# Performance work log

Measured on AMD Instinct MI355X. Metric: run time of the kernel, lower is better.

The kernel has to match this reference:

```python
import jax, jax.numpy as jnp
import numpy as np
import itertools

BINS_NUM = 35
BINS_SIZE = 9
ORDERS = (2, 3, 4, 5)

def _comb_idx(n, k):
    # combinations with replacement of indices 0..n-1, shape [ncomb, k]
    return np.array(list(itertools.combinations_with_replacement(range(n), k)), dtype=np.int32)

_COMB = {k: _comb_idx(BINS_SIZE, k) for k in ORDERS}


def setup_inputs() -> dict:
    key = jax.random.key(0)
    x = jax.random.normal(key, (1024, BINS_NUM * BINS_SIZE), dtype=jnp.float32)
    return {"x": x}


def reference(x) -> jnp.ndarray:
    B = x.shape[0]
    bins = x.reshape(B, BINS_NUM, BINS_SIZE)          # [B, 35, 9]
    parts = [bins]                                     # 'origin' slice first
    for k in ORDERS:
        idx = jnp.asarray(_COMB[k])                    # [ncomb_k, k]
        gathered = bins[:, :, idx]                     # [B, 35, ncomb_k, k]
        parts.append(jnp.prod(gathered, axis=-1))      # [B, 35, ncomb_k]
    # per-bin concat [origin, de2, de3, de4, de5], then flatten bins -> matches
    # torch's outer concat over bins since bin is the leading concat axis here.
    out = jnp.concatenate(parts, axis=-1)              # [B, 35, 2001]
    return out.reshape(B, -1)                          # [B, 70035]
```

## Files before the change

### kernel.cpp

```cpp
#include <hip/hip_runtime.h>

#define BSZ 9
#define NPB 2001
#define N2 45
#define N3 165
#define N4 495
#define O2 9
#define O3 54
#define O4 219
#define ONE_SLOT 714
#define LSZ 720
#define NBLOCKS 1792
#define STRIDE_T (NBLOCKS * 4)

#define WAVE_SYNC() asm volatile("s_waitcnt lgkmcnt(0)" ::: "memory")

typedef float vfloat4 __attribute__((ext_vector_type(4)));

constexpr unsigned pslot2(unsigned i, unsigned j) {
    return O2 + i * 9u - i * (i - 1u) / 2u + (j - i);
}

struct Tabs { unsigned short p2[N2]; unsigned short p3[N3]; unsigned short p4[N4]; };
constexpr Tabs make_tabs() {
    Tabs t{};
    { int p = 0;
      for (unsigned i = 0; i < 9; ++i)
          for (unsigned j = i; j < 9; ++j)
              t.p2[p++] = (unsigned short)(i | (j << 8)); }
    { int p = 0;
      for (unsigned a = 0; a < 9; ++a)
          for (unsigned b = a; b < 9; ++b) {
              const unsigned ps = pslot2(a, b);
              for (unsigned c = b; c < 9; ++c)
                  t.p3[p++] = (unsigned short)(ps | (c << 8));
          } }
    { int p = 0; unsigned ts = O3;
      for (unsigned a = 0; a < 9; ++a)
          for (unsigned b = a; b < 9; ++b)
              for (unsigned c = b; c < 9; ++c) {
                  for (unsigned d = c; d < 9; ++d)
                      t.p4[p++] = (unsigned short)(ts | (d << 8));
                  ++ts;
              } }
    return t;
}
__constant__ Tabs g_tabs = make_tabs();

struct Full { unsigned t[NPB]; };
constexpr Full make_full() {
    Full f{};
    for (unsigned j = 0; j < ONE_SLOT; ++j)
        f.t[j] = (4u * j) | ((4u * ONE_SLOT) << 16);
    { int p = ONE_SLOT; unsigned qs = O4;
      for (unsigned a = 0; a < 9; ++a)
          for (unsigned b = a; b < 9; ++b)
              for (unsigned c = b; c < 9; ++c)
                  for (unsigned d = c; d < 9; ++d) {
                      for (unsigned e = d; e < 9; ++e)
                          f.t[p++] = (4u * qs) | ((4u * e) << 16);
                      ++qs;
                  } }
    return f;
}
__constant__ Full g_full = make_full();

__global__ __launch_bounds__(256) void poly_expand_kernel(
        const float* __restrict__ x, float* __restrict__ out, int ntask) {
    __shared__ float L[4][LSZ];
    const int wave = threadIdx.x >> 6;
    const int lane = threadIdx.x & 63;
    const int w0 = blockIdx.x * 4 + wave;
    if (w0 >= ntask) return;
    float* const Lw = L[wave];

    const unsigned o     = (unsigned)w0 & 3u;
    const unsigned a     = (4u - o) & 3u;
    const unsigned mA    = (ONE_SLOT - a) >> 2;
    const unsigned mB0   = (ONE_SLOT - a + 3u) >> 2;
    const unsigned Mfull = (NPB - a) >> 2;
    float* const Ls = Lw + o;
    const char* const Lc = (const char*)Ls;
    const float* const Afp = Lw + o + a;

    const unsigned t2 = (lane < N2) ? (unsigned)g_tabs.p2[lane] : 0u;
    unsigned t3[3], t4[8];
    #pragma unroll
    for (int k = 0; k < 3; ++k) { const int s = lane + 64 * k;
        t3[k] = (s < N3) ? (unsigned)g_tabs.p3[s] : 0u; }
    #pragma unroll
    for (int k = 0; k < 8; ++k) { const int s = lane + 64 * k;
        t4[k] = (s < N4) ? (unsigned)g_tabs.p4[s] : 0u; }

    const unsigned jb0 = a + 4u * mB0;
    unsigned bpk[6][4];
    #pragma unroll
    for (int k = 0; k < 6; ++k) {
        const unsigned idx = (unsigned)lane + 64u * k;
        #pragma unroll
        for (int e = 0; e < 4; ++e)
            bpk[k][e] = (idx < 321u) ? g_full.t[jb0 + 4u * idx + (unsigned)e] : 0u;
    }

    const unsigned z1s = a + 4u * mA, z1n = 4u * (mB0 - mA);
    const unsigned z2s = a + 4u * Mfull, z2n = (unsigned)NPB - z2s;
    int jm = -1;
    if ((unsigned)lane < a)                 jm = lane;
    else if ((unsigned)lane < a + z1n)      jm = (int)(z1s + ((unsigned)lane - a));
    else if ((unsigned)lane < a + z1n + z2n) jm = (int)(z2s + ((unsigned)lane - a - z1n));
    const unsigned mpk = (jm >= 0) ? g_full.t[jm] : 0u;

    if (lane == 9) Ls[ONE_SLOT] = 1.0f;

    float xreg = 0.0f;
    if (lane < 9) xreg = x[(size_t)w0 * BSZ + lane];

    for (int task = w0; task < ntask; task += STRIDE_T) {
        const unsigned rb = (unsigned)task * (unsigned)NPB;
        WAVE_SYNC();

        if (lane < 9) Ls[lane] = xreg;
        {
            const int nxt = task + STRIDE_T;
            if (lane < 9 && nxt < ntask) xreg = x[(size_t)nxt * BSZ + lane];
        }
        WAVE_SYNC();
        if (lane < N2) Ls[O2 + lane] = Ls[t2 & 255u] * Ls[t2 >> 8];
        WAVE_SYNC();
        #pragma unroll
        for (int k = 0; k < 3; ++k) { const int s = lane + 64 * k;
            if (s < N3) Ls[O3 + s] = Ls[t3[k] & 255u] * Ls[t3[k] >> 8]; }
        WAVE_SYNC();
        #pragma unroll
        for (int k = 0; k < 8; ++k) { const int s = lane + 64 * k;
            if (s < N4) Ls[O4 + s] = Ls[t4[k] & 255u] * Ls[t4[k] >> 8]; }
        WAVE_SYNC();

        float* const po = out + rb + a;

        #pragma unroll
        for (int k = 0; k < 3; ++k) {
            const unsigned m = (unsigned)lane + 64u * k;
            if (m < mA) {
                *(vfloat4*)(po + 4u * m) = *(const vfloat4*)(Afp + 4u * m);
            }
        }
        #pragma unroll
        for (int k = 0; k < 6; ++k) {
            const unsigned idx = (unsigned)lane + 64u * k;
            if (idx < 321u) {
                vfloat4 r;
                #pragma unroll
                for (int e = 0; e < 4; ++e) {
                    const unsigned pk = bpk[k][e];
                    r[e] = *(const float*)(Lc + (pk & 0xFFFFu)) *
                           *(const float*)(Lc + (pk >> 16));
                }
                *(vfloat4*)(po + 4u * (mB0 + idx)) = r;
            }
        }
        if (jm >= 0)
            out[rb + (unsigned)jm] = *(const float*)(Lc + (mpk & 0xFFFFu)) *
                                     *(const float*)(Lc + (mpk >> 16));
    }
}

extern "C" void kernel_launch(void* const* d_in, const int* in_sizes, int n_in,
                              void* d_out, int out_size, void* d_ws, size_t ws_size,
                              hipStream_t stream) {
    const float* x = (const float*)d_in[0];
    float* out = (float*)d_out;
    const int ntask = in_sizes[0] / BSZ;
    int blocks = (ntask + 3) / 4;
    if (blocks > NBLOCKS) blocks = NBLOCKS;
    poly_expand_kernel<<<blocks, 256, 0, stream>>>(x, out, ntask);
}
```

Baseline: 51.83 us.

## Double-buffer LDS tables and overlap next-task products with current output writes

Each wave gets two LDS buffers, so it can build the degree-2/3/4 product tables for the next task while it computes and stores the degree-5 outputs for the current task. This interleaving is meant to hide the serialized LDS table-build phases behind global stores. The fifth-order loop now runs 5 unpredicated groups, and the leftover 1 to 4 elements are moved into the per-lane scalar tail. Costs are twice the LDS per block, LSZ trimmed to 716 to compensate, and more complex indexing.

```diff
diff --git a/kernel.cpp b/kernel.cpp
--- a/kernel.cpp
+++ b/kernel.cpp
@@ -9,7 +9,7 @@
 #define O3 54
 #define O4 219
 #define ONE_SLOT 714
-#define LSZ 720
+#define LSZ 716
 #define NBLOCKS 1792
 #define STRIDE_T (NBLOCKS * 4)
 
@@ -65,23 +65,33 @@
 }
 __constant__ Full g_full = make_full();
 
+#define B_GROUP(KK) do {                                                     \
+    const unsigned idx_ = (unsigned)lane + 64u * (KK);                       \
+    vfloat4 r_;                                                              \
+    _Pragma("unroll")                                                        \
+    for (int e_ = 0; e_ < 4; ++e_) {                                         \
+        const unsigned pk_ = bpk[KK][e_];                                    \
+        r_[e_] = *(const float*)(LcC + (pk_ & 0xFFFFu)) *                    \
+                 *(const float*)(LcC + (pk_ >> 16));                         \
+    }                                                                        \
+    *(vfloat4*)(po + 4u * (mB0 + idx_)) = r_;                                \
+} while (0)
+
 __global__ __launch_bounds__(256) void poly_expand_kernel(
         const float* __restrict__ x, float* __restrict__ out, int ntask) {
-    __shared__ float L[4][LSZ];
+    __shared__ float L[4][2][LSZ];
     const int wave = threadIdx.x >> 6;
     const int lane = threadIdx.x & 63;
     const int w0 = blockIdx.x * 4 + wave;
     if (w0 >= ntask) return;
-    float* const Lw = L[wave];
-
-    const unsigned o     = (unsigned)w0 & 3u;
-    const unsigned a     = (4u - o) & 3u;
-    const unsigned mA    = (ONE_SLOT - a) >> 2;
-    const unsigned mB0   = (ONE_SLOT - a + 3u) >> 2;
+    float* const bufA = &L[wave][0][0];
+    float* const bufB = &L[wave][1][0];
+
+    const unsigned o   = (unsigned)w0 & 3u;
+    const unsigned a   = (4u - o) & 3u;
+    const unsigned mA  = (ONE_SLOT - a) >> 2;
+    const unsigned mB0 = (ONE_SLOT - a + 3u) >> 2;
     const unsigned Mfull = (NPB - a) >> 2;
-    float* const Ls = Lw + o;
-    const char* const Lc = (const char*)Ls;
-    const float* const Afp = Lw + o + a;
 
     const unsigned t2 = (lane < N2) ? (unsigned)g_tabs.p2[lane] : 0u;
     unsigned t3[3], t4[8];
@@ -93,37 +103,37 @@
         t4[k] = (s < N4) ? (unsigned)g_tabs.p4[s] : 0u; }
 
     const unsigned jb0 = a + 4u * mB0;
-    unsigned bpk[6][4];
+    unsigned bpk[5][4];
     #pragma unroll
-    for (int k = 0; k < 6; ++k) {
+    for (int k = 0; k < 5; ++k) {
         const unsigned idx = (unsigned)lane + 64u * k;
         #pragma unroll
         for (int e = 0; e < 4; ++e)
-            bpk[k][e] = (idx < 321u) ? g_full.t[jb0 + 4u * idx + (unsigned)e] : 0u;
-    }
-
-    const unsigned z1s = a + 4u * mA, z1n = 4u * (mB0 - mA);
+            bpk[k][e] = g_full.t[jb0 + 4u * idx + (unsigned)e];
+    }
+
+    const unsigned z1s = a + 4u * mA, z1n = jb0 - z1s;
     const unsigned z2s = a + 4u * Mfull, z2n = (unsigned)NPB - z2s;
     int jm = -1;
-    if ((unsigned)lane < a)                 jm = lane;
-    else if ((unsigned)lane < a + z1n)      jm = (int)(z1s + ((unsigned)lane - a));
-    else if ((unsigned)lane < a + z1n + z2n) jm = (int)(z2s + ((unsigned)lane - a - z1n));
+    {
+        const unsigned l = (unsigned)lane;
+        if (l < a)                         jm = (int)l;
+        else if (l < a + z1n)              jm = (int)(z1s + (l - a));
+        else if (l < a + z1n + z2n)        jm = (int)(z2s + (l - a - z1n));
+        else if (l < a + z1n + z2n + 4u)   jm = (int)(jb0 + 1280u + (l - a - z1n - z2n));
+    }
     const unsigned mpk = (jm >= 0) ? g_full.t[jm] : 0u;
 
-    if (lane == 9) Ls[ONE_SLOT] = 1.0f;
+    if (lane == 9) { bufA[o + ONE_SLOT] = 1.0f; bufB[o + ONE_SLOT] = 1.0f; }
 
     float xreg = 0.0f;
     if (lane < 9) xreg = x[(size_t)w0 * BSZ + lane];
 
-    for (int task = w0; task < ntask; task += STRIDE_T) {
-        const unsigned rb = (unsigned)task * (unsigned)NPB;
-        WAVE_SYNC();
-
+    {
+        float* const Ls = bufA + o;
         if (lane < 9) Ls[lane] = xreg;
-        {
-            const int nxt = task + STRIDE_T;
-            if (lane < 9 && nxt < ntask) xreg = x[(size_t)nxt * BSZ + lane];
-        }
+        { const int nxt = w0 + STRIDE_T;
+          if (lane < 9 && nxt < ntask) xreg = x[(size_t)nxt * BSZ + lane]; }
         WAVE_SYNC();
         if (lane < N2) Ls[O2 + lane] = Ls[t2 & 255u] * Ls[t2 >> 8];
         WAVE_SYNC();
@@ -135,33 +145,57 @@
         for (int k = 0; k < 8; ++k) { const int s = lane + 64 * k;
             if (s < N4) Ls[O4 + s] = Ls[t4[k] & 255u] * Ls[t4[k] >> 8]; }
         WAVE_SYNC();
-
+    }
+
+    float* cur = bufA;
+    float* nxt = bufB;
+    int task = w0;
+    for (;;) {
+        const bool hn = (task + STRIDE_T) < ntask;
+        const unsigned rb = (unsigned)task * (unsigned)NPB;
         float* const po = out + rb + a;
-
+        float* const LsC = cur + o;
+        const char* const LcC = (const char*)LsC;
+        const float* const AfpC = cur + o + a;
+        float* const LsN = nxt + o;
+
+        if (hn && lane < 9) LsN[lane] = xreg;
+        if (hn) { const int n2 = task + 2 * STRIDE_T;
+                  if (lane < 9 && n2 < ntask) xreg = x[(size_t)n2 * BSZ + lane]; }
         #pragma unroll
         for (int k = 0; k < 3; ++k) {
             const unsigned m = (unsigned)lane + 64u * k;
-            if (m < mA) {
-                *(vfloat4*)(po + 4u * m) = *(const vfloat4*)(Afp + 4u * m);
-            }
+            if (m < mA)
+                *(vfloat4*)(po + 4u * m) = *(const vfloat4*)(AfpC + 4u * m);
         }
-        #pragma unroll
-        for (int k = 0; k < 6; ++k) {
-            const unsigned idx = (unsigned)lane + 64u * k;
-            if (idx < 321u) {
-                vfloat4 r;
-                #pragma unroll
-                for (int e = 0; e < 4; ++e) {
-                    const unsigned pk = bpk[k][e];
-                    r[e] = *(const float*)(Lc + (pk & 0xFFFFu)) *
-                           *(const float*)(Lc + (pk >> 16));
-                }
-                *(vfloat4*)(po + 4u * (mB0 + idx)) = r;
-            }
+        WAVE_SYNC();
+
+        if (hn && lane < N2) LsN[O2 + lane] = LsN[t2 & 255u] * LsN[t2 >> 8];
+        B_GROUP(0); B_GROUP(1);
+        WAVE_SYNC();
+
+        if (hn) {
+            #pragma unroll
+            for (int k = 0; k < 3; ++k) { const int s = lane + 64 * k;
+                if (s < N3) LsN[O3 + s] = LsN[t3[k] & 255u] * LsN[t3[k] >> 8]; }
         }
+        B_GROUP(2); B_GROUP(3);
+        WAVE_SYNC();
+
+        if (hn) {
+            #pragma unroll
+            for (int k = 0; k < 8; ++k) { const int s = lane + 64 * k;
+                if (s < N4) LsN[O4 + s] = LsN[t4[k] & 255u] * LsN[t4[k] >> 8]; }
+        }
+        B_GROUP(4);
         if (jm >= 0)
-            out[rb + (unsigned)jm] = *(const float*)(Lc + (mpk & 0xFFFFu)) *
-                                     *(const float*)(Lc + (mpk >> 16));
+            out[rb + (unsigned)jm] = *(const float*)(LcC + (mpk & 0xFFFFu)) *
+                                     *(const float*)(LcC + (mpk >> 16));
+        WAVE_SYNC();
+
+        if (!hn) break;
+        task += STRIDE_T;
+        float* tmp = cur; cur = nxt; nxt = tmp;
     }
 }
 
```

Result: slower. 53.11 us (+2.5%).
